# Performance work log

Measured on AMD Instinct MI355X. Metric: run time of the kernel, lower is better.

## Reference

```python
import jax, jax.numpy as jnp
import numpy as np

N_E = 1024
E_DIM = 64


def setup_inputs() -> dict:
    key = jax.random.key(0)
    k_z, k_emb = jax.random.split(key)
    z = jax.random.normal(k_z, (8, 16, 32, 32, E_DIM), dtype=jnp.float32)
    embeddings = jax.random.normal(k_emb, (N_E, E_DIM), dtype=jnp.float32) * 0.02
    return {"z": z, "embeddings": embeddings}


def reference(z, embeddings):
    # flatten all leading dims: [B*T*H*W, e_dim]
    zf = z.reshape(-1, z.shape[-1])
    # squared L2 distance: ||z||^2 + ||e||^2 - 2 z.e  -> [tokens, n_e]
    d = (jnp.sum(zf ** 2, axis=1, keepdims=True)
         + jnp.sum(embeddings ** 2, axis=1)[None, :]
         - 2.0 * jnp.einsum('bd,nd->bn', zf, embeddings))
    idx = jnp.argmin(d, axis=1)
    z_q = embeddings[idx].reshape(z.shape)
    idx = idx.reshape(z.shape[:-1])
    return z_q, idx
```

## Files before the change

kernel.cpp:

```cpp
#include <hip/hip_runtime.h>

typedef short short8 __attribute__((ext_vector_type(8)));
typedef float f32x4 __attribute__((ext_vector_type(4)));

#define NTOK (8 * 16 * 32 * 32)
#define NE 1024
#define ED 64
#define TPB 256
#define MBLK 256
#define NMF 4
#define WKEY (1 << 19)
#define SCALE (-131072.0f)

__device__ __forceinline__ unsigned short bf16_rtne(float f) {
    unsigned u = __float_as_uint(f);
    return (unsigned short)((u + 0x7FFFu + ((u >> 16) & 1u)) >> 16);
}

__device__ float exact_dist(const float* __restrict__ z, const float* __restrict__ emb,
                            int t, int e) {
    const float* zt = z + (size_t)t * ED;
    const float* ep = emb + (size_t)e * ED;
    float r0 = 0.f, r1 = 0.f, r2 = 0.f, r3 = 0.f;
    float r4 = 0.f, r5 = 0.f, r6 = 0.f, r7 = 0.f;
    for (int d = 0; d < ED; d += 8) {
        r0 += zt[d + 0] * zt[d + 0];
        r1 += zt[d + 1] * zt[d + 1];
        r2 += zt[d + 2] * zt[d + 2];
        r3 += zt[d + 3] * zt[d + 3];
        r4 += zt[d + 4] * zt[d + 4];
        r5 += zt[d + 5] * zt[d + 5];
        r6 += zt[d + 6] * zt[d + 6];
        r7 += zt[d + 7] * zt[d + 7];
    }
    float s1 = ((r0 + r1) + (r2 + r3)) + ((r4 + r5) + (r6 + r7));
    float q0 = 0.f, q1 = 0.f, q2 = 0.f, q3 = 0.f;
    float q4 = 0.f, q5 = 0.f, q6 = 0.f, q7 = 0.f;
    for (int d = 0; d < ED; d += 8) {
        float v0 = ep[d + 0], v1 = ep[d + 1], v2 = ep[d + 2], v3 = ep[d + 3];
        float v4 = ep[d + 4], v5 = ep[d + 5], v6 = ep[d + 6], v7 = ep[d + 7];
        q0 += v0 * v0; q1 += v1 * v1; q2 += v2 * v2; q3 += v3 * v3;
        q4 += v4 * v4; q5 += v5 * v5; q6 += v6 * v6; q7 += v7 * v7;
    }
    float s2 = ((q0 + q1) + (q2 + q3)) + ((q4 + q5) + (q6 + q7));
    float a0 = 0.f, a1 = 0.f, a2 = 0.f, a3 = 0.f;
    for (int d = 0; d < ED; d += 4) {
        a0 = fmaf(zt[d + 0], ep[d + 0], a0);
        a1 = fmaf(zt[d + 1], ep[d + 1], a1);
        a2 = fmaf(zt[d + 2], ep[d + 2], a2);
        a3 = fmaf(zt[d + 3], ep[d + 3], a3);
    }
    float g = (a0 + a1) + (a2 + a3);
    return (s1 + s2) - 2.0f * g;
}

__global__ __launch_bounds__(128) void vq_prep(
    const float* __restrict__ emb,
    unsigned short* __restrict__ bfH,
    float* __restrict__ s2s)
{
    const int f = blockIdx.x * 128 + threadIdx.x;
    const int col = f & 15;
    const int quad = (f >> 4) & 3;
    const int kb = (f >> 6) & 1;
    const int nt = f >> 7;
    const int e = nt * 16 + col;
    const int k0 = kb * 32 + quad * 8;

    const float* p = emb + (size_t)e * ED + k0;
    float4 v0 = *(const float4*)p;
    float4 v1 = *(const float4*)(p + 4);
    float vs[8] = {v0.x, v0.y, v0.z, v0.w, v1.x, v1.y, v1.z, v1.w};
    short8 h;
#pragma unroll
    for (int j = 0; j < 8; ++j) {
        float x = vs[j] * SCALE;
        h[j] = (short)bf16_rtne(x);
    }
    *(short8*)&bfH[(size_t)f * 8] = h;

    if (f < 4096) {
        const int row = f >> 2;
        const float4* rp = (const float4*)(emb + (size_t)row * ED + (f & 3) * 16);
        float4 a = rp[0], b = rp[1], c = rp[2], d = rp[3];
        float s = a.x * a.x + a.y * a.y + a.z * a.z + a.w * a.w
                + b.x * b.x + b.y * b.y + b.z * b.z + b.w * b.w
                + c.x * c.x + c.y * c.y + c.z * c.z + c.w * c.w
                + d.x * d.x + d.y * d.y + d.z * d.z + d.w * d.w;
        s += __shfl_xor(s, 1);
        s += __shfl_xor(s, 2);
        if ((f & 3) == 0) s2s[row] = s * 65536.0f;
    }
}

__global__ void __launch_bounds__(TPB) vq_main(
    const float* __restrict__ z,
    const float* __restrict__ emb,
    const unsigned short* __restrict__ bfH,
    const float* __restrict__ s2s_g,
    float* __restrict__ zq_out,
    float* __restrict__ idx_out)
{
    __shared__ float s2L[NE];
    __shared__ int idx_lds[MBLK];

    const int tid = threadIdx.x;
    const int lane = tid & 63;
    const int wv = __builtin_amdgcn_readfirstlane(tid >> 6);
    const int col = lane & 15;
    const int quad = lane >> 4;
    const int blockTok = blockIdx.x * MBLK;

    for (int i = tid; i < NE; i += TPB) s2L[i] = s2s_g[i];

    short8 Ah[NMF][2];
#pragma unroll
    for (int mf = 0; mf < NMF; ++mf) {
#pragma unroll
        for (int kf = 0; kf < 2; ++kf) {
            const float* zp = z + (size_t)(blockTok + wv * 64 + mf * 16 + col) * ED
                              + kf * 32 + quad * 8;
            float4 v0 = *(const float4*)zp;
            float4 v1 = *(const float4*)(zp + 4);
            float vs[8] = {v0.x, v0.y, v0.z, v0.w, v1.x, v1.y, v1.z, v1.w};
            short8 h;
#pragma unroll
            for (int j = 0; j < 8; ++j) h[j] = (short)bf16_rtne(vs[j]);
            Ah[mf][kf] = h;
        }
    }

    int aK[NMF][4], bK[NMF][4];
#pragma unroll
    for (int mf = 0; mf < NMF; ++mf)
#pragma unroll
        for (int r = 0; r < 4; ++r) { aK[mf][r] = 0x7FFFFFFF; bK[mf][r] = 0x7FFFFFFF; }

    const uint4* u4H = (const uint4*)bfH;

    uint4 cB0a = u4H[lane];
    uint4 cB1a = u4H[64 + lane];
    uint4 cB0b = u4H[128 + lane];
    uint4 cB1b = u4H[192 + lane];

    __syncthreads();

    float s2c0 = s2L[col];
    float s2c1 = s2L[16 + col];

    f32x4 ccPA[NMF], ccPB[NMF];
    {
        short8 BhA0 = __builtin_bit_cast(short8, cB0a);
        short8 BhA1 = __builtin_bit_cast(short8, cB1a);
        short8 BhB0 = __builtin_bit_cast(short8, cB0b);
        short8 BhB1 = __builtin_bit_cast(short8, cB1b);
        __builtin_amdgcn_s_setprio(1);
#pragma unroll
        for (int mf = 0; mf < NMF; ++mf) {
            f32x4 c0 = {s2c0, s2c0, s2c0, s2c0};
            c0 = __builtin_amdgcn_mfma_f32_16x16x32_bf16(Ah[mf][0], BhA0, c0, 0, 0, 0);
            c0 = __builtin_amdgcn_mfma_f32_16x16x32_bf16(Ah[mf][1], BhA1, c0, 0, 0, 0);
            ccPA[mf] = c0;
        }
#pragma unroll
        for (int mf = 0; mf < NMF; ++mf) {
            f32x4 c1 = {s2c1, s2c1, s2c1, s2c1};
            c1 = __builtin_amdgcn_mfma_f32_16x16x32_bf16(Ah[mf][0], BhB0, c1, 0, 0, 0);
            c1 = __builtin_amdgcn_mfma_f32_16x16x32_bf16(Ah[mf][1], BhB1, c1, 0, 0, 0);
            ccPB[mf] = c1;
        }
        __builtin_amdgcn_s_setprio(0);
    }
    cB0a = u4H[256 + lane];
    cB1a = u4H[256 + 64 + lane];
    cB0b = u4H[384 + lane];
    cB1b = u4H[384 + 64 + lane];
    s2c0 = s2L[32 + col];
    s2c1 = s2L[48 + col];

    for (int nt = 2; nt < 64; nt += 2) {
        const int nb2 = (((nt + 2) & 63) << 7) + lane;
        const int nb3 = (((nt + 3) & 63) << 7) + lane;
        uint4 nB0a = u4H[nb2];
        uint4 nB1a = u4H[nb2 + 64];
        uint4 nB0b = u4H[nb3];
        uint4 nB1b = u4H[nb3 + 64];
        float s2n0 = s2L[((nt + 2) & 63) * 16 + col];
        float s2n1 = s2L[((nt + 3) & 63) * 16 + col];

        short8 BhA0 = __builtin_bit_cast(short8, cB0a);
        short8 BhA1 = __builtin_bit_cast(short8, cB1a);
        short8 BhB0 = __builtin_bit_cast(short8, cB0b);
        short8 BhB1 = __builtin_bit_cast(short8, cB1b);

        f32x4 ccCA[NMF], ccCB[NMF];
        __builtin_amdgcn_s_setprio(1);
#pragma unroll
        for (int mf = 0; mf < NMF; ++mf) {
            f32x4 c0 = {s2c0, s2c0, s2c0, s2c0};
            c0 = __builtin_amdgcn_mfma_f32_16x16x32_bf16(Ah[mf][0], BhA0, c0, 0, 0, 0);
            c0 = __builtin_amdgcn_mfma_f32_16x16x32_bf16(Ah[mf][1], BhA1, c0, 0, 0, 0);
            ccCA[mf] = c0;
        }
#pragma unroll
        for (int mf = 0; mf < NMF; ++mf) {
            f32x4 c1 = {s2c1, s2c1, s2c1, s2c1};
            c1 = __builtin_amdgcn_mfma_f32_16x16x32_bf16(Ah[mf][0], BhB0, c1, 0, 0, 0);
            c1 = __builtin_amdgcn_mfma_f32_16x16x32_bf16(Ah[mf][1], BhB1, c1, 0, 0, 0);
            ccCB[mf] = c1;
        }
        __builtin_amdgcn_s_setprio(0);

        const int e0 = (nt - 2) * 16 + col;
        const int e1 = e0 + 16;
#pragma unroll
        for (int mf = 0; mf < NMF; ++mf) {
#pragma unroll
            for (int r = 0; r < 4; ++r) {
                int ci = (int)ccPA[mf][r];
                int key;
                asm("v_mad_i32_i24 %0, %1, %2, %3"
                    : "=v"(key) : "v"(ci), "s"(1024), "v"(e0));
                const int a0 = aK[mf][r];
                int t1 = min(a0, key);
                int med;
                asm("v_med3_i32 %0, %1, %2, %3"
                    : "=v"(med) : "v"(a0), "v"(bK[mf][r]), "v"(key));
                bK[mf][r] = med;
                aK[mf][r] = t1;
            }
        }
#pragma unroll
        for (int mf = 0; mf < NMF; ++mf) {
#pragma unroll
            for (int r = 0; r < 4; ++r) {
                int ci = (int)ccPB[mf][r];
                int key;
                asm("v_mad_i32_i24 %0, %1, %2, %3"
                    : "=v"(key) : "v"(ci), "s"(1024), "v"(e1));
                const int a0 = aK[mf][r];
                int t1 = min(a0, key);
                int med;
                asm("v_med3_i32 %0, %1, %2, %3"
                    : "=v"(med) : "v"(a0), "v"(bK[mf][r]), "v"(key));
                bK[mf][r] = med;
                aK[mf][r] = t1;
            }
        }

#pragma unroll
        for (int mf = 0; mf < NMF; ++mf) { ccPA[mf] = ccCA[mf]; ccPB[mf] = ccCB[mf]; }
        cB0a = nB0a; cB1a = nB1a; cB0b = nB0b; cB1b = nB1b;
        s2c0 = s2n0; s2c1 = s2n1;
    }

    {
        const int e0 = 62 * 16 + col;
        const int e1 = e0 + 16;
#pragma unroll
        for (int mf = 0; mf < NMF; ++mf) {
#pragma unroll
            for (int r = 0; r < 4; ++r) {
                int ci = (int)ccPA[mf][r];
                int key;
                asm("v_mad_i32_i24 %0, %1, %2, %3"
                    : "=v"(key) : "v"(ci), "s"(1024), "v"(e0));
                const int a0 = aK[mf][r];
                int t1 = min(a0, key);
                int med;
                asm("v_med3_i32 %0, %1, %2, %3"
                    : "=v"(med) : "v"(a0), "v"(bK[mf][r]), "v"(key));
                bK[mf][r] = med;
                aK[mf][r] = t1;
            }
        }
#pragma unroll
        for (int mf = 0; mf < NMF; ++mf) {
#pragma unroll
            for (int r = 0; r < 4; ++r) {
                int ci = (int)ccPB[mf][r];
                int key;
                asm("v_mad_i32_i24 %0, %1, %2, %3"
                    : "=v"(key) : "v"(ci), "s"(1024), "v"(e1));
                const int a0 = aK[mf][r];
                int t1 = min(a0, key);
                int med;
                asm("v_med3_i32 %0, %1, %2, %3"
                    : "=v"(med) : "v"(a0), "v"(bK[mf][r]), "v"(key));
                bK[mf][r] = med;
                aK[mf][r] = t1;
            }
        }
    }

#pragma unroll
    for (int mf = 0; mf < NMF; ++mf) {
#pragma unroll
        for (int r = 0; r < 4; ++r) {
            const int a0 = aK[mf][r], b0 = bK[mf][r];
            int A = a0, B = b0;
#pragma unroll
            for (int off = 1; off < 16; off <<= 1) {
                int A2 = __shfl_xor(A, off);
                int B2 = __shfl_xor(B, off);
                int lo = min(A, A2), hi = max(A, A2);
                B = min(min(B, B2), hi);
                A = lo;
            }
            int winner = A & 1023;
            if (B - A <= WKEY) {
                const int t = blockTok + wv * 64 + mf * 16 + quad * 4 + r;
                float dbest = 3.4e38f;
                int ibest = 1 << 30;
                if (a0 <= A + WKEY) {
                    int e = a0 & 1023;
                    float d = exact_dist(z, emb, t, e);
                    if (d < dbest || (d == dbest && e < ibest)) { dbest = d; ibest = e; }
                }
                if (b0 <= A + WKEY) {
                    int e = b0 & 1023;
                    float d = exact_dist(z, emb, t, e);
                    if (d < dbest || (d == dbest && e < ibest)) { dbest = d; ibest = e; }
                }
#pragma unroll
                for (int off = 1; off < 16; off <<= 1) {
                    float d2 = __shfl_xor(dbest, off);
                    int i2 = __shfl_xor(ibest, off);
                    if (d2 < dbest || (d2 == dbest && i2 < ibest)) { dbest = d2; ibest = i2; }
                }
                winner = ibest;
            }
            if (col == 0) idx_lds[wv * 64 + mf * 16 + quad * 4 + r] = winner;
        }
    }

    __syncthreads();

    idx_out[blockTok + tid] = (float)idx_lds[tid];
    const float4* emb_f4 = (const float4*)emb;
    float4* zq_f4 = (float4*)zq_out;
#pragma unroll
    for (int i = 0; i < MBLK * 16 / TPB; ++i) {
        int item = tid + i * TPB;
        int tl = item >> 4, f4 = item & 15;
        int wi = idx_lds[tl];
        zq_f4[(size_t)(blockTok + tl) * 16 + f4] = emb_f4[(size_t)wi * 16 + f4];
    }
}

extern "C" void kernel_launch(void* const* d_in, const int* in_sizes, int n_in,
                              void* d_out, int out_size, void* d_ws, size_t ws_size,
                              hipStream_t stream) {
    const float* z = (const float*)d_in[0];
    const float* emb = (const float*)d_in[1];
    float* out = (float*)d_out;
    float* zq = out;
    float* idx = out + (size_t)NTOK * ED;

    char* ws = (char*)d_ws;
    float* s2s = (float*)ws;
    unsigned short* bfH = (unsigned short*)(ws + 4096);

    vq_prep<<<64, 128, 0, stream>>>(emb, bfH, s2s);
    vq_main<<<NTOK / MBLK, TPB, 0, stream>>>(z, emb, bfH, s2s, zq, idx);
}
```

Before: 129.4 us.

## Split codebook across wave pairs and merge top-2 keys through LDS

Each block now handles 128 tokens instead of 256. Two waves share each 64-token group, and each wave scans half of the codebook. The per-lane top-2 keys are merged across the wave pair through shared memory, and each wave then finishes the reduction and exact re-check for half of the row fragments. This doubles the grid and shortens each wave's serial loop, which should improve occupancy and latency hiding, with launch bounds asking for 4 blocks per CU. The cost is duplicated loading and conversion of z per wave pair, an extra barrier, and extra LDS traffic for the merge.

```diff
diff --git a/kernel.cpp b/kernel.cpp
--- a/kernel.cpp
+++ b/kernel.cpp
@@ -7,7 +7,7 @@
 #define NE 1024
 #define ED 64
 #define TPB 256
-#define MBLK 256
+#define MBLK 128
 #define NMF 4
 #define WKEY (1 << 19)
 #define SCALE (-131072.0f)
@@ -93,7 +93,7 @@
     }
 }
 
-__global__ void __launch_bounds__(TPB) vq_main(
+__global__ void __launch_bounds__(TPB, 4) vq_main(
     const float* __restrict__ z,
     const float* __restrict__ emb,
     const unsigned short* __restrict__ bfH,
@@ -103,13 +103,19 @@
 {
     __shared__ float s2L[NE];
     __shared__ int idx_lds[MBLK];
+    __shared__ int mA[2][2][8][64];
+    __shared__ int mB[2][2][8][64];
 
     const int tid = threadIdx.x;
     const int lane = tid & 63;
     const int wv = __builtin_amdgcn_readfirstlane(tid >> 6);
+    const int grp = wv & 1;
+    const int half = wv >> 1;
     const int col = lane & 15;
     const int quad = lane >> 4;
     const int blockTok = blockIdx.x * MBLK;
+    const int tokBase = blockTok + grp * 64;
+    const int sBase = half * 32;
 
     for (int i = tid; i < NE; i += TPB) s2L[i] = s2s_g[i];
 
@@ -118,7 +124,7 @@
     for (int mf = 0; mf < NMF; ++mf) {
 #pragma unroll
         for (int kf = 0; kf < 2; ++kf) {
-            const float* zp = z + (size_t)(blockTok + wv * 64 + mf * 16 + col) * ED
+            const float* zp = z + (size_t)(tokBase + mf * 16 + col) * ED
                               + kf * 32 + quad * 8;
             float4 v0 = *(const float4*)zp;
             float4 v1 = *(const float4*)(zp + 4);
@@ -138,15 +144,15 @@
 
     const uint4* u4H = (const uint4*)bfH;
 
-    uint4 cB0a = u4H[lane];
-    uint4 cB1a = u4H[64 + lane];
-    uint4 cB0b = u4H[128 + lane];
-    uint4 cB1b = u4H[192 + lane];
+    uint4 cB0a = u4H[(sBase << 7) + lane];
+    uint4 cB1a = u4H[(sBase << 7) + 64 + lane];
+    uint4 cB0b = u4H[((sBase + 1) << 7) + lane];
+    uint4 cB1b = u4H[((sBase + 1) << 7) + 64 + lane];
 
     __syncthreads();
 
-    float s2c0 = s2L[col];
-    float s2c1 = s2L[16 + col];
+    float s2c0 = s2L[sBase * 16 + col];
+    float s2c1 = s2L[(sBase + 1) * 16 + col];
 
     f32x4 ccPA[NMF], ccPB[NMF];
     {
@@ -171,22 +177,22 @@
         }
         __builtin_amdgcn_s_setprio(0);
     }
-    cB0a = u4H[256 + lane];
-    cB1a = u4H[256 + 64 + lane];
-    cB0b = u4H[384 + lane];
-    cB1b = u4H[384 + 64 + lane];
-    s2c0 = s2L[32 + col];
-    s2c1 = s2L[48 + col];
-
-    for (int nt = 2; nt < 64; nt += 2) {
-        const int nb2 = (((nt + 2) & 63) << 7) + lane;
-        const int nb3 = (((nt + 3) & 63) << 7) + lane;
-        uint4 nB0a = u4H[nb2];
-        uint4 nB1a = u4H[nb2 + 64];
-        uint4 nB0b = u4H[nb3];
-        uint4 nB1b = u4H[nb3 + 64];
-        float s2n0 = s2L[((nt + 2) & 63) * 16 + col];
-        float s2n1 = s2L[((nt + 3) & 63) * 16 + col];
+    cB0a = u4H[((sBase + 2) << 7) + lane];
+    cB1a = u4H[((sBase + 2) << 7) + 64 + lane];
+    cB0b = u4H[((sBase + 3) << 7) + lane];
+    cB1b = u4H[((sBase + 3) << 7) + 64 + lane];
+    s2c0 = s2L[(sBase + 2) * 16 + col];
+    s2c1 = s2L[(sBase + 3) * 16 + col];
+
+    for (int it = 1; it < 16; ++it) {
+        const int ntc = sBase + 2 * it;
+        const int ntn = sBase + ((2 * it + 2) & 31);
+        uint4 nB0a = u4H[(ntn << 7) + lane];
+        uint4 nB1a = u4H[(ntn << 7) + 64 + lane];
+        uint4 nB0b = u4H[((ntn + 1) << 7) + lane];
+        uint4 nB1b = u4H[((ntn + 1) << 7) + 64 + lane];
+        float s2n0 = s2L[ntn * 16 + col];
+        float s2n1 = s2L[(ntn + 1) * 16 + col];
 
         short8 BhA0 = __builtin_bit_cast(short8, cB0a);
         short8 BhA1 = __builtin_bit_cast(short8, cB1a);
@@ -211,7 +217,7 @@
         }
         __builtin_amdgcn_s_setprio(0);
 
-        const int e0 = (nt - 2) * 16 + col;
+        const int e0 = (ntc - 2) * 16 + col;
         const int e1 = e0 + 16;
 #pragma unroll
         for (int mf = 0; mf < NMF; ++mf) {
@@ -255,7 +261,7 @@
     }
 
     {
-        const int e0 = 62 * 16 + col;
+        const int e0 = (sBase + 30) * 16 + col;
         const int e1 = e0 + 16;
 #pragma unroll
         for (int mf = 0; mf < NMF; ++mf) {
@@ -293,8 +299,33 @@
         }
     }
 
-#pragma unroll
-    for (int mf = 0; mf < NMF; ++mf) {
+    {
+        const int wbase = 2 * (1 - half);
+#pragma unroll
+        for (int m = 0; m < 2; ++m)
+#pragma unroll
+            for (int r = 0; r < 4; ++r) {
+                mA[grp][half][m * 4 + r][lane] = aK[wbase + m][r];
+                mB[grp][half][m * 4 + r][lane] = bK[wbase + m][r];
+            }
+    }
+    __syncthreads();
+
+    const int rbase = 2 * half;
+#pragma unroll
+    for (int m = 0; m < 2; ++m)
+#pragma unroll
+        for (int r = 0; r < 4; ++r) {
+            const int ao = mA[grp][1 - half][m * 4 + r][lane];
+            const int bo = mB[grp][1 - half][m * 4 + r][lane];
+            const int as = aK[rbase + m][r], bs = bK[rbase + m][r];
+            aK[rbase + m][r] = min(as, ao);
+            bK[rbase + m][r] = min(max(as, ao), min(bs, bo));
+        }
+
+#pragma unroll
+    for (int m = 0; m < 2; ++m) {
+        const int mf = rbase + m;
 #pragma unroll
         for (int r = 0; r < 4; ++r) {
             const int a0 = aK[mf][r], b0 = bK[mf][r];
@@ -309,7 +340,7 @@
             }
             int winner = A & 1023;
             if (B - A <= WKEY) {
-                const int t = blockTok + wv * 64 + mf * 16 + quad * 4 + r;
+                const int t = tokBase + mf * 16 + quad * 4 + r;
                 float dbest = 3.4e38f;
                 int ibest = 1 << 30;
                 if (a0 <= A + WKEY) {
@@ -330,13 +361,13 @@
                 }
                 winner = ibest;
             }
-            if (col == 0) idx_lds[wv * 64 + mf * 16 + quad * 4 + r] = winner;
+            if (col == 0) idx_lds[grp * 64 + mf * 16 + quad * 4 + r] = winner;
         }
     }
 
     __syncthreads();
 
-    idx_out[blockTok + tid] = (float)idx_lds[tid];
+    if (tid < MBLK) idx_out[blockTok + tid] = (float)idx_lds[tid];
     const float4* emb_f4 = (const float4*)emb;
     float4* zq_f4 = (float4*)zq_out;
 #pragma unroll
```

Result: slower. 316.6 us (+144.6%).
